# Kernel tuning notes

Measured on AMD Instinct MI355X. Metric: run time of the kernel, lower is better.

## Reference

```python
import jax, jax.numpy as jnp
import numpy as np

B, S, H, E = 8, 2048, 1024, 8

def setup_inputs() -> dict:
    key = jax.random.key(0)
    ks = jax.random.split(key, 7)
    sc = 1.0 / np.sqrt(H)
    return {
        "x":   jax.random.normal(ks[0], (B, S, H), dtype=jnp.float32),
        "We":  jax.random.normal(ks[1], (E, H, H), dtype=jnp.float32) * sc,
        "be":  jax.random.normal(ks[2], (E, H), dtype=jnp.float32) * 0.01,
        "Wr1": jax.random.normal(ks[3], (H, H), dtype=jnp.float32) * sc,
        "br1": jax.random.normal(ks[4], (H,), dtype=jnp.float32) * 0.01,
        "Wr2": jax.random.normal(ks[5], (H, E), dtype=jnp.float32) * sc,
        "br2": jax.random.normal(ks[6], (E,), dtype=jnp.float32) * 0.01,
    }

def reference(x, We, be, Wr1, br1, Wr2, br2):
    # Router: mean over seq -> Linear+ReLU -> Linear -> softmax over experts
    x_mean = x.mean(axis=1)                                   # [B,H]
    h = jax.nn.relu(x_mean @ Wr1 + br1)                        # [B,H]
    routing = jax.nn.softmax(h @ Wr2 + br2, axis=-1)           # [B,E]
    # Dense all-experts MLP: every expert processes every token
    eo = jax.nn.relu(jnp.einsum('bsh,ehd->ebsd', x, We)
                     + be[:, None, None, :])                   # [E,B,S,H]
    # KV caches are zero-initialized and read before any update in the
    # original forward, so their additive contribution is zero here.
    out = jnp.einsum('ebsd,be->bsd', eo, routing)              # [B,S,H]
    return out
```

## Files before the change

kernel.cpp:

```cpp
#include <hip/hip_runtime.h>
#include <stdint.h>

#define Hdim 1024
#define Bdim 8
#define Sdim 2048
#define Edim 8
#define Mtot 16384
#define Ntot 8192

typedef short bf16x8 __attribute__((ext_vector_type(8)));
typedef unsigned short u16x8 __attribute__((ext_vector_type(8)));
typedef float f32x4 __attribute__((ext_vector_type(4)));

__device__ __forceinline__ unsigned short f2bf(float f) {
  union { float f; unsigned u; } v; v.f = f;
  unsigned r = (v.u + 0x7FFFu + ((v.u >> 16) & 1u)) >> 16;
  return (unsigned short)r;
}

__device__ __forceinline__ void gload16(const void* g, void* l) {
  __builtin_amdgcn_global_load_lds((const __attribute__((address_space(1))) void*)g,
                                   (__attribute__((address_space(3))) void*)l,
                                   16, 0, 0);
}

#define VMCNT_(N) asm volatile("s_waitcnt vmcnt(" #N ")" ::: "memory")
#define VMCNT(N) VMCNT_(N)

__global__ void k_convert_mean(const float* __restrict__ x,
                               unsigned short* __restrict__ xb,
                               float* __restrict__ part) {
  const int b = blockIdx.y;
  const int s0 = blockIdx.x * 32;
  const int t = threadIdx.x;
  const int hg = (t & 127) << 3;
  const int sp = t >> 7;
  float accv[8];
#pragma unroll
  for (int q = 0; q < 8; ++q) accv[q] = 0.f;
#pragma unroll 4
  for (int i = 0; i < 16; ++i) {
    const int s = s0 + sp + (i << 1);
    const size_t base = ((size_t)b * Sdim + s) * Hdim + hg;
    const float4 lo = *(const float4*)(x + base);
    const float4 hi = *(const float4*)(x + base + 4);
    accv[0] += lo.x; accv[1] += lo.y; accv[2] += lo.z; accv[3] += lo.w;
    accv[4] += hi.x; accv[5] += hi.y; accv[6] += hi.z; accv[7] += hi.w;
    u16x8 pk;
    pk[0] = f2bf(lo.x); pk[1] = f2bf(lo.y); pk[2] = f2bf(lo.z); pk[3] = f2bf(lo.w);
    pk[4] = f2bf(hi.x); pk[5] = f2bf(hi.y); pk[6] = f2bf(hi.z); pk[7] = f2bf(hi.w);
    *(u16x8*)(xb + base) = pk;
  }
  float* pp = part + ((size_t)b * 128 + blockIdx.x * 2 + sp) * Hdim + hg;
#pragma unroll
  for (int q = 0; q < 8; ++q) pp[q] = accv[q];
}

__global__ void k_transpose_w(const float* __restrict__ We,
                              unsigned short* __restrict__ wt) {
  __shared__ float lds[64][65];
  const int e = blockIdx.z, hb = blockIdx.y, db = blockIdx.x;
  const int t = threadIdx.x;
  const float* src = We + ((size_t)e * Hdim + hb * 64) * Hdim + db * 64;
#pragma unroll 4
  for (int it = 0; it < 16; ++it) {
    int idx = it * 256 + t;
    int r = idx >> 6, c = idx & 63;
    lds[r][c] = src[(size_t)r * Hdim + c];
  }
  __syncthreads();
#pragma unroll 4
  for (int it = 0; it < 16; ++it) {
    int idx = it * 256 + t;
    int r = idx >> 6, c = idx & 63;
    const int np = (db * 64 + r) * 8 + e;
    wt[(size_t)np * Hdim + hb * 64 + c] = f2bf(lds[c][r]);
  }
}

__global__ void k_router1(const float* __restrict__ part,
                          const float* __restrict__ Wr1,
                          const float* __restrict__ br1,
                          float* __restrict__ hbuf) {
  __shared__ float xm[Hdim];
  const int b = blockIdx.y, jc = blockIdx.x, t = threadIdx.x;
  for (int k = t; k < Hdim; k += 256) {
    float s = 0.f;
    const float* p = part + (size_t)b * 128 * Hdim + k;
#pragma unroll 8
    for (int c = 0; c < 128; ++c) s += p[(size_t)c * Hdim];
    xm[k] = s * (1.0f / 2048.0f);
  }
  __syncthreads();
  const int j = jc * 256 + t;
  float acc = br1[j];
#pragma unroll 8
  for (int k = 0; k < Hdim; ++k) acc = fmaf(xm[k], Wr1[(size_t)k * Hdim + j], acc);
  hbuf[b * Hdim + j] = fmaxf(acc, 0.f);
}

__global__ void k_router2(const float* __restrict__ hbuf,
                          const float* __restrict__ Wr2,
                          const float* __restrict__ br2,
                          float* __restrict__ routing) {
  const int t = threadIdx.x;
  const int e = t & 7;
  const int b = t >> 3;
  float acc = br2[e];
  const float* hb = hbuf + b * Hdim;
#pragma unroll 8
  for (int k = 0; k < Hdim; ++k) acc = fmaf(hb[k], Wr2[k * Edim + e], acc);
  float m = acc;
  for (int d = 1; d < 8; d <<= 1) m = fmaxf(m, __shfl_xor(m, d, 64));
  float p = __expf(acc - m);
  float s = p;
  for (int d = 1; d < 8; d <<= 1) s += __shfl_xor(s, d, 64);
  routing[t] = p / s;
}

__global__ __launch_bounds__(512, 2)
void k_moe_gemm(const unsigned short* __restrict__ xb,
                const unsigned short* __restrict__ wt,
                const float* __restrict__ be,
                const float* __restrict__ routing,
                float* __restrict__ out) {
  extern __shared__ char smem[];
  const int t = threadIdx.x;
  const int wave = t >> 6, lane = t & 63;
  const int la15 = lane & 15;
  const int wr = wave >> 2;
  const int wcn = wave & 3;

  const int bid = blockIdx.x;
  const int wg = (bid & 7) * 256 + (bid >> 3);
  const int m0 = (wg >> 5) * 256;
  const int n0 = (wg & 31) * 256;

  const int rr0 = t >> 2;
  const int cs = (((t & 3) ^ ((rr0 >> 1) & 3)) << 3);
  const unsigned short* aSrc0 = xb + (size_t)(m0 + rr0) * Hdim + cs;
  const unsigned short* bSrc0 = wt + (size_t)(n0 + rr0) * Hdim + cs;
  char* ldsA = smem;
  char* ldsB = smem + 65536;
  const int woff = wave * 1024;

  const int swz = (((lane >> 4) ^ ((la15 >> 1) & 3)) << 4);
  const int aRdOff = (wr * 128 + la15) * 64 + swz;
  const int bRdOff = (wcn * 64 + la15) * 64 + swz;

  f32x4 acc[8][4];
#pragma unroll
  for (int i = 0; i < 8; ++i)
#pragma unroll
    for (int j = 0; j < 4; ++j) acc[i][j] = (f32x4){0.f, 0.f, 0.f, 0.f};

#define STAGE(pt) { \
    const int buf_ = (pt) & 3; const int k0_ = (pt) * 32; \
    gload16(aSrc0 + k0_,               ldsA + buf_ * 16384 + woff); \
    gload16(aSrc0 + 128 * Hdim + k0_,  ldsA + buf_ * 16384 + 8192 + woff); \
    gload16(bSrc0 + k0_,               ldsB + buf_ * 16384 + woff); \
    gload16(bSrc0 + 128 * Hdim + k0_,  ldsB + buf_ * 16384 + 8192 + woff); \
  }

#define PHASE_BODY(p, DO_STAGE) { \
    const char* ra_ = smem + ((p) & 3) * 16384 + aRdOff; \
    const char* rb_ = smem + 65536 + ((p) & 3) * 16384 + bRdOff; \
    bf16x8 af[8]; bf16x8 bf[4]; \
    _Pragma("unroll") for (int i_ = 0; i_ < 8; ++i_) af[i_] = *(const bf16x8*)(ra_ + i_ * 1024); \
    _Pragma("unroll") for (int j_ = 0; j_ < 4; ++j_) bf[j_] = *(const bf16x8*)(rb_ + j_ * 1024); \
    if (DO_STAGE) STAGE((p) + 3); \
    __builtin_amdgcn_s_barrier(); \
    asm volatile("s_waitcnt lgkmcnt(0)" ::: "memory"); \
    __builtin_amdgcn_s_setprio(1); \
    _Pragma("unroll") for (int i_ = 0; i_ < 8; ++i_) \
      _Pragma("unroll") for (int j_ = 0; j_ < 4; ++j_) \
        acc[i_][j_] = __builtin_amdgcn_mfma_f32_16x16x32_bf16(af[i_], bf[j_], acc[i_][j_], 0, 0, 0); \
    __builtin_amdgcn_s_setprio(0); \
  }

  STAGE(0); STAGE(1); STAGE(2);
  VMCNT(8);
  __builtin_amdgcn_s_barrier();

#pragma unroll 4
  for (int p = 0; p < 28; ++p) {
    PHASE_BODY(p, 1);
    VMCNT(8);
    __builtin_amdgcn_s_barrier();
  }
  PHASE_BODY(28, 1);
  VMCNT(8);
  __builtin_amdgcn_s_barrier();
  PHASE_BODY(29, 0);
  VMCNT(4);
  __builtin_amdgcn_s_barrier();
  PHASE_BODY(30, 0);
  VMCNT(0);
  __builtin_amdgcn_s_barrier();
  PHASE_BODY(31, 0);
  __builtin_amdgcn_s_barrier();

  float* outb = (float*)smem;
  const int bidx = m0 >> 11;
  const float rw = routing[bidx * Edim + (lane & 7)];
  const int dblk = (lane >> 3) & 1;
  const bool writer = ((lane & 7) == 0);
#pragma unroll
  for (int j = 0; j < 4; ++j) {
    const int col0 = wcn * 64 + j * 16;
    const float bias = be[(lane & 7) * Hdim + (n0 >> 3) + (col0 >> 3) + dblk];
#pragma unroll
    for (int i = 0; i < 8; ++i) {
#pragma unroll
      for (int r = 0; r < 4; ++r) {
        float v = fmaxf(acc[i][j][r] + bias, 0.f) * rw;
        v += __shfl_xor(v, 1, 64);
        v += __shfl_xor(v, 2, 64);
        v += __shfl_xor(v, 4, 64);
        if (writer) {
          const int row = wr * 128 + i * 16 + ((lane >> 4) << 2) + r;
          outb[row * 33 + (col0 >> 3) + dblk] = v;
        }
      }
    }
  }
  __builtin_amdgcn_s_barrier();
  const size_t obase = (size_t)m0 * Hdim + (n0 >> 3);
#pragma unroll
  for (int it = 0; it < 4; ++it) {
    const int r = it * 64 + (t >> 3);
    const int c = (t & 7) * 4;
    float4 vv;
    vv.x = outb[r * 33 + c];
    vv.y = outb[r * 33 + c + 1];
    vv.z = outb[r * 33 + c + 2];
    vv.w = outb[r * 33 + c + 3];
    *(float4*)(out + obase + (size_t)r * Hdim + c) = vv;
  }
#undef STAGE
#undef PHASE_BODY
}

extern "C" void kernel_launch(void* const* d_in, const int* in_sizes, int n_in,
                              void* d_out, int out_size, void* d_ws, size_t ws_size,
                              hipStream_t stream) {
  const float* x   = (const float*)d_in[0];
  const float* We  = (const float*)d_in[1];
  const float* be  = (const float*)d_in[2];
  const float* Wr1 = (const float*)d_in[3];
  const float* br1 = (const float*)d_in[4];
  const float* Wr2 = (const float*)d_in[5];
  const float* br2 = (const float*)d_in[6];
  float* out = (float*)d_out;

  char* ws = (char*)d_ws;
  unsigned short* xb = (unsigned short*)ws;
  unsigned short* wt = (unsigned short*)(ws + 33554432);
  float* part    = (float*)(ws + 50331648);
  float* hbuf    = (float*)(ws + 54525952);
  float* routing = (float*)(ws + 54558720);

  hipFuncSetAttribute((const void*)k_moe_gemm,
                      hipFuncAttributeMaxDynamicSharedMemorySize, 131072);

  k_convert_mean<<<dim3(Sdim / 32, Bdim), 256, 0, stream>>>(x, xb, part);
  k_transpose_w<<<dim3(Hdim / 64, Hdim / 64, Edim), 256, 0, stream>>>(We, wt);
  k_router1<<<dim3(Hdim / 256, Bdim), 256, 0, stream>>>(part, Wr1, br1, hbuf);
  k_router2<<<1, 64, 0, stream>>>(hbuf, Wr2, br2, routing);
  k_moe_gemm<<<dim3(2048), 512, 131072, stream>>>(xb, wt, be, routing, out);
}
```

Measured before the change: 481.9 us.

## Restructure MoE GEMM main loop into 8-phase quadrant pipeline with BK=64 double buffer

Replaces the 4-deep BK=32 ring buffer with a 2-buffer BK=64 layout and splits each K-tile into quadrant sub-phases. Each sub-phase interleaves LDS fragment loads, one quarter-tile global-to-LDS stage, and a block of MFMAs, in a ping-pong schedule similar to hipBLASLt-style 256x256 kernels. The aim is finer overlap of global loads with MFMA work and fewer long stalls per tile. The cost is more barriers per K step, a new XOR swizzle over 128-byte rows, and extra register pressure from holding two A and two B fragment sets.

```diff
diff --git a/kernel.cpp b/kernel.cpp
--- a/kernel.cpp
+++ b/kernel.cpp
@@ -26,6 +26,7 @@
 
 #define VMCNT_(N) asm volatile("s_waitcnt vmcnt(" #N ")" ::: "memory")
 #define VMCNT(N) VMCNT_(N)
+#define BAR() __builtin_amdgcn_s_barrier()
 
 __global__ void k_convert_mean(const float* __restrict__ x,
                                unsigned short* __restrict__ xb,
@@ -136,17 +137,17 @@
   const int m0 = (wg >> 5) * 256;
   const int n0 = (wg & 31) * 256;
 
-  const int rr0 = t >> 2;
-  const int cs = (((t & 3) ^ ((rr0 >> 1) & 3)) << 3);
-  const unsigned short* aSrc0 = xb + (size_t)(m0 + rr0) * Hdim + cs;
-  const unsigned short* bSrc0 = wt + (size_t)(n0 + rr0) * Hdim + cs;
-  char* ldsA = smem;
-  char* ldsB = smem + 65536;
-  const int woff = wave * 1024;
-
-  const int swz = (((lane >> 4) ^ ((la15 >> 1) & 3)) << 4);
-  const int aRdOff = (wr * 128 + la15) * 64 + swz;
-  const int bRdOff = (wcn * 64 + la15) * 64 + swz;
+  const int cx = (((lane & 7) ^ (lane >> 3)) << 3);
+  const unsigned short* aStage = xb + (size_t)(m0 + wave * 8 + (lane >> 3)) * Hdim + cx;
+  const int bRowLoc = ((wave & 3) << 3) + ((wave >> 2) << 6) + (lane >> 3);
+  const unsigned short* bStage = wt + (size_t)(n0 + bRowLoc) * Hdim + cx;
+  const int aLdsW = wave * 1024;
+  const int bLdsW = ((wave & 3) << 10) + ((wave >> 2) << 13);
+
+  const int swz0 = (((lane >> 4) ^ (lane & 7)) << 4);
+  const int swz1 = ((((lane >> 4) + 4) ^ (lane & 7)) << 4);
+  const int aRd = (wr * 128 + la15) * 128;
+  const int bRd = (wcn * 64 + la15) * 128;
 
   f32x4 acc[8][4];
 #pragma unroll
@@ -154,51 +155,69 @@
 #pragma unroll
     for (int j = 0; j < 4; ++j) acc[i][j] = (f32x4){0.f, 0.f, 0.f, 0.f};
 
-#define STAGE(pt) { \
-    const int buf_ = (pt) & 3; const int k0_ = (pt) * 32; \
-    gload16(aSrc0 + k0_,               ldsA + buf_ * 16384 + woff); \
-    gload16(aSrc0 + 128 * Hdim + k0_,  ldsA + buf_ * 16384 + 8192 + woff); \
-    gload16(bSrc0 + k0_,               ldsB + buf_ * 16384 + woff); \
-    gload16(bSrc0 + 128 * Hdim + k0_,  ldsB + buf_ * 16384 + 8192 + woff); \
-  }
-
-#define PHASE_BODY(p, DO_STAGE) { \
-    const char* ra_ = smem + ((p) & 3) * 16384 + aRdOff; \
-    const char* rb_ = smem + 65536 + ((p) & 3) * 16384 + bRdOff; \
-    bf16x8 af[8]; bf16x8 bf[4]; \
-    _Pragma("unroll") for (int i_ = 0; i_ < 8; ++i_) af[i_] = *(const bf16x8*)(ra_ + i_ * 1024); \
-    _Pragma("unroll") for (int j_ = 0; j_ < 4; ++j_) bf[j_] = *(const bf16x8*)(rb_ + j_ * 1024); \
-    if (DO_STAGE) STAGE((p) + 3); \
-    __builtin_amdgcn_s_barrier(); \
-    asm volatile("s_waitcnt lgkmcnt(0)" ::: "memory"); \
+#define STG_A(half, buf, k0) do { \
+    gload16(aStage + (half) * 64 * 1024 + (k0),          smem + (buf) * 32768 + aLdsW + (half) * 8192); \
+    gload16(aStage + (128 + (half) * 64) * 1024 + (k0),  smem + (buf) * 32768 + aLdsW + 16384 + (half) * 8192); \
+  } while (0)
+#define STG_B(sub, buf, k0) do { \
+    gload16(bStage + (sub) * 32 * 1024 + (k0),           smem + 65536 + (buf) * 32768 + bLdsW + (sub) * 4096); \
+    gload16(bStage + (128 + (sub) * 32) * 1024 + (k0),   smem + 65536 + (buf) * 32768 + bLdsW + 16384 + (sub) * 4096); \
+  } while (0)
+#define LD_A(dst, buf, qi) do { \
+    _Pragma("unroll") for (int ii = 0; ii < 4; ++ii) { \
+      dst[ii][0] = *(const bf16x8*)(smem + (buf) * 32768 + aRd + (qi) * 8192 + ii * 2048 + swz0); \
+      dst[ii][1] = *(const bf16x8*)(smem + (buf) * 32768 + aRd + (qi) * 8192 + ii * 2048 + swz1); } \
+  } while (0)
+#define LD_B(dst, buf, qj) do { \
+    _Pragma("unroll") for (int jj = 0; jj < 2; ++jj) { \
+      dst[jj][0] = *(const bf16x8*)(smem + 65536 + (buf) * 32768 + bRd + (qj) * 4096 + jj * 2048 + swz0); \
+      dst[jj][1] = *(const bf16x8*)(smem + 65536 + (buf) * 32768 + bRd + (qj) * 4096 + jj * 2048 + swz1); } \
+  } while (0)
+#define MF_Q(af_, bf_, qi, jh) do { \
     __builtin_amdgcn_s_setprio(1); \
-    _Pragma("unroll") for (int i_ = 0; i_ < 8; ++i_) \
-      _Pragma("unroll") for (int j_ = 0; j_ < 4; ++j_) \
-        acc[i_][j_] = __builtin_amdgcn_mfma_f32_16x16x32_bf16(af[i_], bf[j_], acc[i_][j_], 0, 0, 0); \
+    _Pragma("unroll") for (int ii = 0; ii < 4; ++ii) \
+      _Pragma("unroll") for (int jj = 0; jj < 2; ++jj) { \
+        acc[(qi)*4+ii][(jh)*2+jj] = __builtin_amdgcn_mfma_f32_16x16x32_bf16(af_[ii][0], bf_[jj][0], acc[(qi)*4+ii][(jh)*2+jj], 0, 0, 0); \
+        acc[(qi)*4+ii][(jh)*2+jj] = __builtin_amdgcn_mfma_f32_16x16x32_bf16(af_[ii][1], bf_[jj][1], acc[(qi)*4+ii][(jh)*2+jj], 0, 0, 0); } \
     __builtin_amdgcn_s_setprio(0); \
-  }
-
-  STAGE(0); STAGE(1); STAGE(2);
+  } while (0)
+
+  STG_A(0, 0, 0);
+  STG_B(0, 0, 0);
+  STG_B(1, 0, 0);
+  STG_A(1, 0, 0);
+  STG_A(0, 1, 64);
+  STG_B(0, 1, 64);
+  STG_B(1, 1, 64);
   VMCNT(8);
-  __builtin_amdgcn_s_barrier();
-
-#pragma unroll 4
-  for (int p = 0; p < 28; ++p) {
-    PHASE_BODY(p, 1);
-    VMCNT(8);
-    __builtin_amdgcn_s_barrier();
-  }
-  PHASE_BODY(28, 1);
-  VMCNT(8);
-  __builtin_amdgcn_s_barrier();
-  PHASE_BODY(29, 0);
-  VMCNT(4);
-  __builtin_amdgcn_s_barrier();
-  PHASE_BODY(30, 0);
+  BAR();
+
+#pragma unroll 1
+  for (int j = 0; j < 8; ++j) {
+    const int kt1 = j * 128 + 64;
+    const int kc2 = (j * 128 + 128) & 1023;
+    const int kc3 = (j * 128 + 192) & 1023;
+    bf16x8 afA[4][2], afB[4][2], bf0[2][2], bf1[2][2];
+    VMCNT(8); LD_A(afA, 0, 0); LD_B(bf0, 0, 0); STG_A(1, 1, kt1);
+    BAR(); MF_Q(afA, bf0, 0, 0); BAR();
+    VMCNT(8); LD_B(bf1, 0, 1); STG_A(0, 0, kc2);
+    BAR(); MF_Q(afA, bf1, 0, 1); BAR();
+    VMCNT(8); LD_A(afB, 0, 1); STG_B(0, 0, kc2);
+    BAR(); MF_Q(afB, bf1, 1, 1); BAR();
+    VMCNT(8); STG_B(1, 0, kc2);
+    BAR(); MF_Q(afB, bf0, 1, 0); BAR();
+    VMCNT(8); LD_A(afA, 1, 0); LD_B(bf0, 1, 0); STG_A(1, 0, kc2);
+    BAR(); MF_Q(afA, bf0, 0, 0); BAR();
+    VMCNT(8); LD_B(bf1, 1, 1); STG_A(0, 1, kc3);
+    BAR(); MF_Q(afA, bf1, 0, 1); BAR();
+    VMCNT(8); LD_A(afB, 1, 1); STG_B(0, 1, kc3);
+    BAR(); MF_Q(afB, bf1, 1, 1); BAR();
+    VMCNT(8); STG_B(1, 1, kc3);
+    BAR(); MF_Q(afB, bf0, 1, 0); BAR();
+  }
+
   VMCNT(0);
-  __builtin_amdgcn_s_barrier();
-  PHASE_BODY(31, 0);
-  __builtin_amdgcn_s_barrier();
+  BAR();
 
   float* outb = (float*)smem;
   const int bidx = m0 >> 11;
@@ -224,7 +243,7 @@
       }
     }
   }
-  __builtin_amdgcn_s_barrier();
+  BAR();
   const size_t obase = (size_t)m0 * Hdim + (n0 >> 3);
 #pragma unroll
   for (int it = 0; it < 4; ++it) {
@@ -237,8 +256,11 @@
     vv.w = outb[r * 33 + c + 3];
     *(float4*)(out + obase + (size_t)r * Hdim + c) = vv;
   }
-#undef STAGE
-#undef PHASE_BODY
+#undef STG_A
+#undef STG_B
+#undef LD_A
+#undef LD_B
+#undef MF_Q
 }
 
 extern "C" void kernel_launch(void* const* d_in, const int* in_sizes, int n_in,
```

New measurement: 462.2 us. -4.1%, faster.
